# Kernel optimization log

Measured on AMD Instinct MI355X. Metric: run time of the kernel, lower is better.

## Reference

```python
import jax, jax.numpy as jnp
import numpy as np

L, B, D, H = 512, 128, 512, 512

def setup_inputs() -> dict:
    key = jax.random.key(0)
    ks = jax.random.split(key, 6)
    s = 1.0 / np.sqrt(H)
    return {
        "x": jax.random.normal(ks[0], (L, B, D), dtype=jnp.float32),
        "h": jax.random.normal(ks[1], (B, H), dtype=jnp.float32),
        "Wx_w": jax.random.normal(ks[2], (H, D), dtype=jnp.float32) * s,
        "Wx_b": jax.random.normal(ks[3], (H,), dtype=jnp.float32) * s,
        "Wh_w": jax.random.normal(ks[4], (H, H), dtype=jnp.float32) * s,
        "Wh_b": jax.random.normal(ks[5], (H,), dtype=jnp.float32) * s,
    }

def reference(x, h, Wx_w, Wx_b, Wh_w, Wh_b):
    # Precompute input projection for all timesteps in one big GEMM:
    # Wx(x_t) + bx + bh  -> [L, B, H]
    xproj = jnp.einsum('lbd,hd->lbh', x, Wx_w) + Wx_b + Wh_b

    def step(h, xp_t):
        # h_t = tanh(Wx(x_t) + Wh(h_{t-1}))
        h_new = jnp.tanh(xp_t + h @ Wh_w.T)
        return h_new, h_new

    h_last, hAll = jax.lax.scan(step, h, xproj)
    return hAll, h_last
```

## Files before the change

### kernel.cpp

```cpp
#include <hip/hip_runtime.h>
#include <math.h>

#define Lt 512
#define Bn 128
#define Dd 512
#define Hh 512
#define BH (Bn * Hh)

typedef __attribute__((ext_vector_type(4))) float f32x4;
typedef __attribute__((ext_vector_type(8))) __bf16 bf16x8;
typedef __attribute__((ext_vector_type(8))) unsigned short u16x8;
typedef __attribute__((ext_vector_type(4))) unsigned int u32x4;

#define MFMA16 __builtin_amdgcn_mfma_f32_16x16x32_bf16

__device__ __forceinline__ float bf2f(unsigned short s) {
    return __uint_as_float(((unsigned)s) << 16);
}
__device__ __forceinline__ unsigned short f2bf_rne(float f) {
    unsigned u = __float_as_uint(f);
    u = (u + 0x7FFFu + ((u >> 16) & 1u)) >> 16;
    return (unsigned short)u;
}
__device__ __forceinline__ float tanh_fast(float z) {
    float e = __expf(2.f * z);
    return 1.f - 2.f * __builtin_amdgcn_rcpf(e + 1.f);
}
__device__ __forceinline__ unsigned pack_hi16(unsigned a, unsigned b) {
    return __builtin_amdgcn_perm(b, a, 0x07060302u);
}
__device__ __forceinline__ unsigned pack_lo16(unsigned a, unsigned b) {
    return __builtin_amdgcn_perm(b, a, 0x05040100u);
}
__device__ __forceinline__ int swzi(int r_, int k_) {
    return (r_ << 9) + (k_ ^ ((r_ & 7) << 3));
}

__global__ void zero_flags_kernel(unsigned* __restrict__ flags) {
    int i = blockIdx.x * 256 + threadIdx.x;
    if (i < 256) flags[i] = 0;
}

__device__ __forceinline__ void preload_w(const float* __restrict__ W, int row,
                                          int quad, bf16x8* wH, bf16x8* wL) {
    const float* wr = W + (size_t)row * 512;
    #pragma unroll
    for (int c = 0; c < 16; ++c) {
        int kk = c * 32 + quad * 8;
        float4 v0 = *(const float4*)(wr + kk);
        float4 v1 = *(const float4*)(wr + kk + 4);
        float vv[8] = {v0.x, v0.y, v0.z, v0.w, v1.x, v1.y, v1.z, v1.w};
        u16x8 hh, ll;
        #pragma unroll
        for (int e = 0; e < 8; ++e) {
            unsigned short s = f2bf_rne(vv[e]);
            hh[e] = s;
            ll[e] = f2bf_rne(vv[e] - bf2f(s));
        }
        wH[c] = __builtin_bit_cast(bf16x8, hh);
        wL[c] = __builtin_bit_cast(bf16x8, ll);
    }
}

__global__ __launch_bounds__(256, 2) void xproj_kernel(
    const float* __restrict__ x, const float* __restrict__ Wx,
    const float* __restrict__ bx, const float* __restrict__ bh,
    float* __restrict__ out) {

    __shared__ unsigned short XH[16 * 512], XL[16 * 512];

    const int tid = threadIdx.x;
    const int wave = tid >> 6;
    const int lane = tid & 63;
    const int rw = lane & 15;
    const int quad = (lane >> 4) & 3;
    const int jgrp = blockIdx.x >> 6;
    const int mslab = blockIdx.x & 63;
    const int j0 = (jgrp * 4 + wave) * 16;

    bf16x8 wxH[16], wxL[16];
    preload_w(Wx, j0 + rw, quad, wxH, wxL);
    const float bsum = bx[j0 + rw] + bh[j0 + rw];

    const int r = tid >> 4;
    const int cf0 = (tid & 15) * 32;

    for (int it = 0; it < 64; ++it) {
        const int m0 = mslab * 1024 + it * 16;
        {
            const float* xr = x + (size_t)(m0 + r) * Dd + cf0;
            float4 v[8];
            #pragma unroll
            for (int q = 0; q < 8; ++q) v[q] = *(const float4*)(xr + q * 4);
            #pragma unroll
            for (int g = 0; g < 4; ++g) {
                float4 va = v[2 * g], vb = v[2 * g + 1];
                unsigned ua0 = __float_as_uint(va.x), ua1 = __float_as_uint(va.y);
                unsigned ua2 = __float_as_uint(va.z), ua3 = __float_as_uint(va.w);
                unsigned ub0 = __float_as_uint(vb.x), ub1 = __float_as_uint(vb.y);
                unsigned ub2 = __float_as_uint(vb.z), ub3 = __float_as_uint(vb.w);
                u32x4 Hq = {pack_hi16(ua0, ua1), pack_hi16(ua2, ua3),
                            pack_hi16(ub0, ub1), pack_hi16(ub2, ub3)};
                float l0 = va.x - __uint_as_float(ua0 & 0xFFFF0000u);
                float l1 = va.y - __uint_as_float(ua1 & 0xFFFF0000u);
                float l2 = va.z - __uint_as_float(ua2 & 0xFFFF0000u);
                float l3 = va.w - __uint_as_float(ua3 & 0xFFFF0000u);
                float l4 = vb.x - __uint_as_float(ub0 & 0xFFFF0000u);
                float l5 = vb.y - __uint_as_float(ub1 & 0xFFFF0000u);
                float l6 = vb.z - __uint_as_float(ub2 & 0xFFFF0000u);
                float l7 = vb.w - __uint_as_float(ub3 & 0xFFFF0000u);
                u32x4 Lq = {pack_hi16(__float_as_uint(l0), __float_as_uint(l1)),
                            pack_hi16(__float_as_uint(l2), __float_as_uint(l3)),
                            pack_hi16(__float_as_uint(l4), __float_as_uint(l5)),
                            pack_hi16(__float_as_uint(l6), __float_as_uint(l7))};
                int idx = swzi(r, cf0 + g * 8);
                *(u32x4*)&XH[idx] = Hq;
                *(u32x4*)&XL[idx] = Lq;
            }
        }
        __syncthreads();
        f32x4 aHH = {0.f, 0.f, 0.f, 0.f};
        f32x4 aHL = {0.f, 0.f, 0.f, 0.f};
        f32x4 aLH = {0.f, 0.f, 0.f, 0.f};
        #pragma unroll
        for (int c = 0; c < 16; ++c) {
            int kk = c * 32 + quad * 8;
            bf16x8 aH = __builtin_bit_cast(bf16x8, *(const u16x8*)&XH[swzi(rw, kk)]);
            bf16x8 aL = __builtin_bit_cast(bf16x8, *(const u16x8*)&XL[swzi(rw, kk)]);
            aHH = MFMA16(aH, wxH[c], aHH, 0, 0, 0);
            aHL = MFMA16(aH, wxL[c], aHL, 0, 0, 0);
            aLH = MFMA16(aL, wxH[c], aLH, 0, 0, 0);
        }
        f32x4 acc = aHH + aHL + aLH;
        #pragma unroll
        for (int rr = 0; rr < 4; ++rr) {
            int m = m0 + quad * 4 + rr;
            out[(size_t)m * Hh + (j0 + rw)] = acc[rr] + bsum;
        }
        __syncthreads();
    }
}

__global__ __launch_bounds__(256, 1) void rnn_rec4_kernel(
    const float* __restrict__ h0in, const float* __restrict__ Wh,
    float* __restrict__ out, unsigned* __restrict__ hpk, unsigned* flags) {

    __shared__ unsigned short HHi[16 * 512], HLo[16 * 512];

    const int tid = threadIdx.x;
    const int wave = tid >> 6;
    const int lane = tid & 63;
    const int rw = lane & 15;
    const int quad = (lane >> 4) & 3;
    const int bg = blockIdx.x & 7;
    const int jgrp = blockIdx.x >> 3;
    const int b0 = bg * 16;
    const int j0 = (jgrp * 4 + wave) * 16;

    bf16x8 whH[16], whL[16];
    preload_w(Wh, j0 + rw, quad, whH, whL);

    #pragma unroll
    for (int rr = 0; rr < 4; ++rr) {
        int b = b0 + quad * 4 + rr;
        float v = h0in[(size_t)b * Hh + (j0 + rw)];
        unsigned u = __float_as_uint(v);
        unsigned hb = u >> 16;
        unsigned lb = __float_as_uint(v - __uint_as_float(u & 0xFFFF0000u)) >> 16;
        __hip_atomic_store(hpk + BH + (size_t)b * Hh + (j0 + rw), (hb << 16) | lb,
                           __ATOMIC_RELAXED, __HIP_MEMORY_SCOPE_AGENT);
    }
    asm volatile("s_waitcnt vmcnt(0)" ::: "memory");
    __syncthreads();
    if (tid == 0) {
        __hip_atomic_store(&flags[bg * 8 + jgrp], 1u, __ATOMIC_RELAXED,
                           __HIP_MEMORY_SCOPE_AGENT);
    }

    const int r = tid >> 4;
    const int c0 = (tid & 15) * 32;

    for (int t = 0; t < Lt; ++t) {
        {
            const unsigned tgt = (unsigned)t + 1u;
            while (true) {
                unsigned v = __hip_atomic_load(&flags[bg * 8 + (lane & 7)],
                                               __ATOMIC_RELAXED,
                                               __HIP_MEMORY_SCOPE_AGENT);
                if (__ballot(v >= tgt) == 0xFFFFFFFFFFFFFFFFull) break;
            }
        }

        float xpv[4];
        {
            const float* xr = out + (size_t)t * BH;
            #pragma unroll
            for (int rr = 0; rr < 4; ++rr)
                xpv[rr] = xr[(size_t)(b0 + quad * 4 + rr) * Hh + (j0 + rw)];
        }

        {
            const unsigned* hrow = hpk + (size_t)((t + 1) & 1) * BH +
                                   (size_t)(b0 + r) * Hh + c0;
            unsigned long long p[16];
            #pragma unroll
            for (int q = 0; q < 16; ++q)
                p[q] = __hip_atomic_load((const unsigned long long*)(hrow + 2 * q),
                                         __ATOMIC_RELAXED,
                                         __HIP_MEMORY_SCOPE_AGENT);
            #pragma unroll
            for (int g = 0; g < 4; ++g) {
                u32x4 Hq, Lq;
                #pragma unroll
                for (int e = 0; e < 4; ++e) {
                    unsigned a = (unsigned)p[g * 4 + e];
                    unsigned b = (unsigned)(p[g * 4 + e] >> 32);
                    Hq[e] = pack_hi16(a, b);
                    Lq[e] = pack_lo16(a, b);
                }
                int idx = swzi(r, c0 + g * 8);
                *(u32x4*)&HHi[idx] = Hq;
                *(u32x4*)&HLo[idx] = Lq;
            }
        }
        __syncthreads();

        f32x4 aHH = {0.f, 0.f, 0.f, 0.f};
        f32x4 aHL = {0.f, 0.f, 0.f, 0.f};
        f32x4 aLH = {0.f, 0.f, 0.f, 0.f};
        #pragma unroll
        for (int c = 0; c < 16; ++c) {
            int kk = c * 32 + quad * 8;
            bf16x8 aH = __builtin_bit_cast(bf16x8, *(const u16x8*)&HHi[swzi(rw, kk)]);
            bf16x8 aL = __builtin_bit_cast(bf16x8, *(const u16x8*)&HLo[swzi(rw, kk)]);
            aHH = MFMA16(aH, whH[c], aHH, 0, 0, 0);
            aHL = MFMA16(aH, whL[c], aHL, 0, 0, 0);
            aLH = MFMA16(aL, whH[c], aLH, 0, 0, 0);
        }
        f32x4 acc = aHH + aHL + aLH;

        float hv[4];
        #pragma unroll
        for (int rr = 0; rr < 4; ++rr) hv[rr] = tanh_fast(acc[rr] + xpv[rr]);

        unsigned* hw = hpk + (size_t)(t & 1) * BH;
        #pragma unroll
        for (int rr = 0; rr < 4; ++rr) {
            int b = b0 + quad * 4 + rr;
            unsigned u = __float_as_uint(hv[rr]);
            unsigned hb = u >> 16;
            unsigned lb =
                __float_as_uint(hv[rr] - __uint_as_float(u & 0xFFFF0000u)) >> 16;
            __hip_atomic_store(hw + (size_t)b * Hh + (j0 + rw), (hb << 16) | lb,
                               __ATOMIC_RELAXED, __HIP_MEMORY_SCOPE_AGENT);
        }
        asm volatile("s_waitcnt vmcnt(0)" ::: "memory");
        __syncthreads();
        if (tid == 0 && t + 1 < Lt) {
            __hip_atomic_store(&flags[bg * 8 + jgrp], (unsigned)(t + 2),
                               __ATOMIC_RELAXED, __HIP_MEMORY_SCOPE_AGENT);
        }

        #pragma unroll
        for (int rr = 0; rr < 4; ++rr) {
            int b = b0 + quad * 4 + rr;
            out[((size_t)t * Bn + b) * Hh + (j0 + rw)] = hv[rr];
        }
        if (t == Lt - 1) {
            #pragma unroll
            for (int rr = 0; rr < 4; ++rr) {
                int b = b0 + quad * 4 + rr;
                out[(size_t)Lt * BH + (size_t)b * Hh + (j0 + rw)] = hv[rr];
            }
        }
    }
}

extern "C" void kernel_launch(void* const* d_in, const int* in_sizes, int n_in,
                              void* d_out, int out_size, void* d_ws, size_t ws_size,
                              hipStream_t stream) {
    const float* x    = (const float*)d_in[0];
    const float* h0   = (const float*)d_in[1];
    const float* Wx_w = (const float*)d_in[2];
    const float* Wx_b = (const float*)d_in[3];
    const float* Wh_w = (const float*)d_in[4];
    const float* Wh_b = (const float*)d_in[5];
    float* out = (float*)d_out;

    unsigned* hpk   = (unsigned*)d_ws;
    unsigned* flags = hpk + 2 * BH;

    zero_flags_kernel<<<1, 256, 0, stream>>>(flags);
    xproj_kernel<<<512, 256, 0, stream>>>(x, Wx_w, Wx_b, Wh_b, out);
    rnn_rec4_kernel<<<64, 256, 0, stream>>>(h0, Wh_w, out, hpk, flags);
}
```

Before: 2.578 ms.

## Restructure recurrence into single-wave blocks loading h directly into registers

The recurrent kernel moves from 64 blocks of four waves to 128 single-wave blocks, each computing two 16-column tiles of the hidden state. Each wave loads the packed h slice straight from global memory into MFMA operands, which removes the LDS staging and both __syncthreads per timestep. The next step's input projection is prefetched after the current step's stores, taking that load off the critical path. In exchange there are twice as many blocks polling flags, 16 flags per batch group instead of 8, and more register pressure from holding weights for two column tiles.

```diff
diff --git a/kernel.cpp b/kernel.cpp
--- a/kernel.cpp
+++ b/kernel.cpp
@@ -37,8 +37,8 @@
 }
 
 __global__ void zero_flags_kernel(unsigned* __restrict__ flags) {
-    int i = blockIdx.x * 256 + threadIdx.x;
-    if (i < 256) flags[i] = 0;
+    int i = threadIdx.x;
+    if (i < 128) flags[i] = 0u;
 }
 
 __device__ __forceinline__ void preload_w(const float* __restrict__ W, int row,
@@ -141,136 +141,175 @@
     }
 }
 
-__global__ __launch_bounds__(256, 1) void rnn_rec4_kernel(
+__global__ __launch_bounds__(64, 1) void rnn_rec2j_kernel(
     const float* __restrict__ h0in, const float* __restrict__ Wh,
-    float* __restrict__ out, unsigned* __restrict__ hpk, unsigned* flags) {
-
-    __shared__ unsigned short HHi[16 * 512], HLo[16 * 512];
-
-    const int tid = threadIdx.x;
-    const int wave = tid >> 6;
-    const int lane = tid & 63;
+    float* __restrict__ out, unsigned* __restrict__ hpk,
+    unsigned* __restrict__ flags) {
+
+    const int lane = threadIdx.x;
+    const int bg = blockIdx.x & 7;
+    const int jg2 = blockIdx.x >> 3;
+    const int b0 = bg * 16;
     const int rw = lane & 15;
-    const int quad = (lane >> 4) & 3;
-    const int bg = blockIdx.x & 7;
-    const int jgrp = blockIdx.x >> 3;
-    const int b0 = bg * 16;
-    const int j0 = (jgrp * 4 + wave) * 16;
-
-    bf16x8 whH[16], whL[16];
-    preload_w(Wh, j0 + rw, quad, whH, whL);
+    const int quad = lane >> 4;
+    const int jA = jg2 * 32;
+    const int jB = jA + 16;
+
+    bf16x8 wAH[16], wAL[16], wBH[16], wBL[16];
+    preload_w(Wh, jA + rw, quad, wAH, wAL);
+    preload_w(Wh, jB + rw, quad, wBH, wBL);
+
+    unsigned* myflag = flags + bg * 16 + jg2;
 
     #pragma unroll
     for (int rr = 0; rr < 4; ++rr) {
         int b = b0 + quad * 4 + rr;
-        float v = h0in[(size_t)b * Hh + (j0 + rw)];
-        unsigned u = __float_as_uint(v);
-        unsigned hb = u >> 16;
-        unsigned lb = __float_as_uint(v - __uint_as_float(u & 0xFFFF0000u)) >> 16;
-        __hip_atomic_store(hpk + BH + (size_t)b * Hh + (j0 + rw), (hb << 16) | lb,
-                           __ATOMIC_RELAXED, __HIP_MEMORY_SCOPE_AGENT);
+        {
+            float v = h0in[(size_t)b * Hh + (jA + rw)];
+            unsigned u = __float_as_uint(v);
+            unsigned hb = u >> 16;
+            unsigned lb = __float_as_uint(v - __uint_as_float(u & 0xFFFF0000u)) >> 16;
+            __hip_atomic_store(hpk + BH + (size_t)b * Hh + (jA + rw),
+                               (hb << 16) | lb, __ATOMIC_RELAXED,
+                               __HIP_MEMORY_SCOPE_AGENT);
+        }
+        {
+            float v = h0in[(size_t)b * Hh + (jB + rw)];
+            unsigned u = __float_as_uint(v);
+            unsigned hb = u >> 16;
+            unsigned lb = __float_as_uint(v - __uint_as_float(u & 0xFFFF0000u)) >> 16;
+            __hip_atomic_store(hpk + BH + (size_t)b * Hh + (jB + rw),
+                               (hb << 16) | lb, __ATOMIC_RELAXED,
+                               __HIP_MEMORY_SCOPE_AGENT);
+        }
     }
     asm volatile("s_waitcnt vmcnt(0)" ::: "memory");
-    __syncthreads();
-    if (tid == 0) {
-        __hip_atomic_store(&flags[bg * 8 + jgrp], 1u, __ATOMIC_RELAXED,
+    if (lane == 0) {
+        __hip_atomic_store(myflag, 1u, __ATOMIC_RELAXED,
                            __HIP_MEMORY_SCOPE_AGENT);
     }
 
-    const int r = tid >> 4;
-    const int c0 = (tid & 15) * 32;
+    float xpA[4], xpB[4];
+    {
+        const float* xr = out;
+        #pragma unroll
+        for (int rr = 0; rr < 4; ++rr) {
+            int b = b0 + quad * 4 + rr;
+            xpA[rr] = xr[(size_t)b * Hh + (jA + rw)];
+            xpB[rr] = xr[(size_t)b * Hh + (jB + rw)];
+        }
+    }
 
     for (int t = 0; t < Lt; ++t) {
         {
             const unsigned tgt = (unsigned)t + 1u;
+            const unsigned* fp = flags + bg * 16 + (lane & 15);
             while (true) {
-                unsigned v = __hip_atomic_load(&flags[bg * 8 + (lane & 7)],
-                                               __ATOMIC_RELAXED,
+                unsigned v = __hip_atomic_load(fp, __ATOMIC_RELAXED,
                                                __HIP_MEMORY_SCOPE_AGENT);
                 if (__ballot(v >= tgt) == 0xFFFFFFFFFFFFFFFFull) break;
             }
         }
 
-        float xpv[4];
-        {
-            const float* xr = out + (size_t)t * BH;
-            #pragma unroll
-            for (int rr = 0; rr < 4; ++rr)
-                xpv[rr] = xr[(size_t)(b0 + quad * 4 + rr) * Hh + (j0 + rw)];
-        }
-
-        {
-            const unsigned* hrow = hpk + (size_t)((t + 1) & 1) * BH +
-                                   (size_t)(b0 + r) * Hh + c0;
-            unsigned long long p[16];
-            #pragma unroll
-            for (int q = 0; q < 16; ++q)
-                p[q] = __hip_atomic_load((const unsigned long long*)(hrow + 2 * q),
-                                         __ATOMIC_RELAXED,
-                                         __HIP_MEMORY_SCOPE_AGENT);
-            #pragma unroll
-            for (int g = 0; g < 4; ++g) {
-                u32x4 Hq, Lq;
-                #pragma unroll
-                for (int e = 0; e < 4; ++e) {
-                    unsigned a = (unsigned)p[g * 4 + e];
-                    unsigned b = (unsigned)(p[g * 4 + e] >> 32);
-                    Hq[e] = pack_hi16(a, b);
-                    Lq[e] = pack_lo16(a, b);
-                }
-                int idx = swzi(r, c0 + g * 8);
-                *(u32x4*)&HHi[idx] = Hq;
-                *(u32x4*)&HLo[idx] = Lq;
-            }
-        }
-        __syncthreads();
-
-        f32x4 aHH = {0.f, 0.f, 0.f, 0.f};
-        f32x4 aHL = {0.f, 0.f, 0.f, 0.f};
-        f32x4 aLH = {0.f, 0.f, 0.f, 0.f};
+        f32x4 aAHH = {0.f, 0.f, 0.f, 0.f};
+        f32x4 aAHL = {0.f, 0.f, 0.f, 0.f};
+        f32x4 aALH = {0.f, 0.f, 0.f, 0.f};
+        f32x4 aBHH = {0.f, 0.f, 0.f, 0.f};
+        f32x4 aBHL = {0.f, 0.f, 0.f, 0.f};
+        f32x4 aBLH = {0.f, 0.f, 0.f, 0.f};
+        const unsigned* hrow =
+            hpk + (size_t)((t + 1) & 1) * BH + (size_t)(b0 + rw) * Hh;
         #pragma unroll
         for (int c = 0; c < 16; ++c) {
             int kk = c * 32 + quad * 8;
-            bf16x8 aH = __builtin_bit_cast(bf16x8, *(const u16x8*)&HHi[swzi(rw, kk)]);
-            bf16x8 aL = __builtin_bit_cast(bf16x8, *(const u16x8*)&HLo[swzi(rw, kk)]);
-            aHH = MFMA16(aH, whH[c], aHH, 0, 0, 0);
-            aHL = MFMA16(aH, whL[c], aHL, 0, 0, 0);
-            aLH = MFMA16(aL, whH[c], aLH, 0, 0, 0);
-        }
-        f32x4 acc = aHH + aHL + aLH;
-
-        float hv[4];
-        #pragma unroll
-        for (int rr = 0; rr < 4; ++rr) hv[rr] = tanh_fast(acc[rr] + xpv[rr]);
+            unsigned long long p0 = __hip_atomic_load(
+                (const unsigned long long*)(hrow + kk + 0),
+                __ATOMIC_RELAXED, __HIP_MEMORY_SCOPE_AGENT);
+            unsigned long long p1 = __hip_atomic_load(
+                (const unsigned long long*)(hrow + kk + 2),
+                __ATOMIC_RELAXED, __HIP_MEMORY_SCOPE_AGENT);
+            unsigned long long p2 = __hip_atomic_load(
+                (const unsigned long long*)(hrow + kk + 4),
+                __ATOMIC_RELAXED, __HIP_MEMORY_SCOPE_AGENT);
+            unsigned long long p3 = __hip_atomic_load(
+                (const unsigned long long*)(hrow + kk + 6),
+                __ATOMIC_RELAXED, __HIP_MEMORY_SCOPE_AGENT);
+            unsigned q0 = (unsigned)p0, q1 = (unsigned)(p0 >> 32);
+            unsigned q2 = (unsigned)p1, q3 = (unsigned)(p1 >> 32);
+            unsigned q4 = (unsigned)p2, q5 = (unsigned)(p2 >> 32);
+            unsigned q6 = (unsigned)p3, q7 = (unsigned)(p3 >> 32);
+            u32x4 hi4 = {pack_hi16(q0, q1), pack_hi16(q2, q3),
+                         pack_hi16(q4, q5), pack_hi16(q6, q7)};
+            u32x4 lo4 = {pack_lo16(q0, q1), pack_lo16(q2, q3),
+                         pack_lo16(q4, q5), pack_lo16(q6, q7)};
+            bf16x8 aH = __builtin_bit_cast(bf16x8, hi4);
+            bf16x8 aL = __builtin_bit_cast(bf16x8, lo4);
+            aAHH = MFMA16(aH, wAH[c], aAHH, 0, 0, 0);
+            aAHL = MFMA16(aH, wAL[c], aAHL, 0, 0, 0);
+            aALH = MFMA16(aL, wAH[c], aALH, 0, 0, 0);
+            aBHH = MFMA16(aH, wBH[c], aBHH, 0, 0, 0);
+            aBHL = MFMA16(aH, wBL[c], aBHL, 0, 0, 0);
+            aBLH = MFMA16(aL, wBH[c], aBLH, 0, 0, 0);
+        }
+        f32x4 accA = aAHH + aAHL + aALH;
+        f32x4 accB = aBHH + aBHL + aBLH;
+
+        float hvA[4], hvB[4];
+        #pragma unroll
+        for (int rr = 0; rr < 4; ++rr) {
+            hvA[rr] = tanh_fast(accA[rr] + xpA[rr]);
+            hvB[rr] = tanh_fast(accB[rr] + xpB[rr]);
+        }
 
         unsigned* hw = hpk + (size_t)(t & 1) * BH;
         #pragma unroll
         for (int rr = 0; rr < 4; ++rr) {
             int b = b0 + quad * 4 + rr;
-            unsigned u = __float_as_uint(hv[rr]);
-            unsigned hb = u >> 16;
-            unsigned lb =
-                __float_as_uint(hv[rr] - __uint_as_float(u & 0xFFFF0000u)) >> 16;
-            __hip_atomic_store(hw + (size_t)b * Hh + (j0 + rw), (hb << 16) | lb,
-                               __ATOMIC_RELAXED, __HIP_MEMORY_SCOPE_AGENT);
+            {
+                unsigned u = __float_as_uint(hvA[rr]);
+                unsigned hb = u >> 16;
+                unsigned lb = __float_as_uint(hvA[rr] -
+                                __uint_as_float(u & 0xFFFF0000u)) >> 16;
+                __hip_atomic_store(hw + (size_t)b * Hh + (jA + rw),
+                                   (hb << 16) | lb, __ATOMIC_RELAXED,
+                                   __HIP_MEMORY_SCOPE_AGENT);
+            }
+            {
+                unsigned u = __float_as_uint(hvB[rr]);
+                unsigned hb = u >> 16;
+                unsigned lb = __float_as_uint(hvB[rr] -
+                                __uint_as_float(u & 0xFFFF0000u)) >> 16;
+                __hip_atomic_store(hw + (size_t)b * Hh + (jB + rw),
+                                   (hb << 16) | lb, __ATOMIC_RELAXED,
+                                   __HIP_MEMORY_SCOPE_AGENT);
+            }
         }
         asm volatile("s_waitcnt vmcnt(0)" ::: "memory");
-        __syncthreads();
-        if (tid == 0 && t + 1 < Lt) {
-            __hip_atomic_store(&flags[bg * 8 + jgrp], (unsigned)(t + 2),
-                               __ATOMIC_RELAXED, __HIP_MEMORY_SCOPE_AGENT);
+        if (lane == 0 && t + 1 < Lt) {
+            __hip_atomic_store(myflag, (unsigned)(t + 2), __ATOMIC_RELAXED,
+                               __HIP_MEMORY_SCOPE_AGENT);
         }
 
         #pragma unroll
         for (int rr = 0; rr < 4; ++rr) {
             int b = b0 + quad * 4 + rr;
-            out[((size_t)t * Bn + b) * Hh + (j0 + rw)] = hv[rr];
-        }
-        if (t == Lt - 1) {
+            out[((size_t)t * Bn + b) * Hh + (jA + rw)] = hvA[rr];
+            out[((size_t)t * Bn + b) * Hh + (jB + rw)] = hvB[rr];
+        }
+        if (t + 1 < Lt) {
+            const float* xr = out + (size_t)(t + 1) * BH;
             #pragma unroll
             for (int rr = 0; rr < 4; ++rr) {
                 int b = b0 + quad * 4 + rr;
-                out[(size_t)Lt * BH + (size_t)b * Hh + (j0 + rw)] = hv[rr];
+                xpA[rr] = xr[(size_t)b * Hh + (jA + rw)];
+                xpB[rr] = xr[(size_t)b * Hh + (jB + rw)];
+            }
+        } else {
+            #pragma unroll
+            for (int rr = 0; rr < 4; ++rr) {
+                int b = b0 + quad * 4 + rr;
+                out[(size_t)Lt * BH + (size_t)b * Hh + (jA + rw)] = hvA[rr];
+                out[(size_t)Lt * BH + (size_t)b * Hh + (jB + rw)] = hvB[rr];
             }
         }
     }
@@ -290,7 +329,7 @@
     unsigned* hpk   = (unsigned*)d_ws;
     unsigned* flags = hpk + 2 * BH;
 
-    zero_flags_kernel<<<1, 256, 0, stream>>>(flags);
+    zero_flags_kernel<<<1, 128, 0, stream>>>(flags);
     xproj_kernel<<<512, 256, 0, stream>>>(x, Wx_w, Wx_b, Wh_b, out);
-    rnn_rec4_kernel<<<64, 256, 0, stream>>>(h0, Wh_w, out, hpk, flags);
-}
+    rnn_rec2j_kernel<<<128, 64, 0, stream>>>(h0, Wh_w, out, hpk, flags);
+}
```

Measured after the change: 4.639 ms. +79.9%, slower.
